# Kernel optimization log

Hardware: AMD Instinct MI355X
Metric: run time of the kernel (lower is better)

## Reference

```python
import jax, jax.numpy as jnp
import numpy as np

B, C, H, W, K = 8, 256, 128, 128, 9
P = K // 2
DN = ('NCHW', 'OIHW', 'NCHW')


def _dw(x, w, pad):
    # depthwise conv: w has shape (C,1,kh,kw), feature_group_count=C
    return jax.lax.conv_general_dilated(
        x, w, window_strides=(1, 1), padding=pad,
        dimension_numbers=DN, feature_group_count=C)


def setup_inputs() -> dict:
    key = jax.random.key(0)
    ks = jax.random.split(key, 6)
    s = 1.0 / np.sqrt(K)
    return {
        'x': jax.random.normal(ks[0], (B, C, H, W), dtype=jnp.float32),
        'wh1': jax.random.normal(ks[1], (C, 1, 1, K), dtype=jnp.float32) * s,
        'wh2': jax.random.normal(ks[2], (C, 1, 1, K), dtype=jnp.float32) * s,
        'wv1': jax.random.normal(ks[3], (C, 1, K, 1), dtype=jnp.float32) * s,
        'wv2': jax.random.normal(ks[4], (C, 1, K, 1), dtype=jnp.float32) * s,
        'wproj': jax.random.normal(ks[5], (C, 4 * C), dtype=jnp.float32) / np.sqrt(4 * C),
    }


def reference(x, wh1, wh2, wv1, wv2, wproj):
    pad_h = ((0, 0), (P, P))  # 1xK conv pads width
    pad_v = ((P, P), (0, 0))  # Kx1 conv pads height
    y = jnp.concatenate([
        _dw(x, wh1, pad_h),
        _dw(x, wh2, pad_h),
        _dw(x, wv1, pad_v),
        _dw(x, wv2, pad_v),
    ], axis=1)  # (B, 4C, H, W)
    out = jnp.einsum('oc,bchw->bohw', wproj, y)  # 1x1 projection
    return jax.nn.relu(out)
```

## Files before the change

### kernel.cpp

```cpp
#include <hip/hip_runtime.h>
#include <hip/hip_bf16.h>

#define BB 8
#define CC 256
#define HH 128
#define WW 128
#define KS 9
#define PADR 4
#define NPIX (BB*HH*WW)
#define KDIM (4*CC)

typedef __attribute__((ext_vector_type(8))) short bf16x8;
typedef __attribute__((ext_vector_type(4))) float f32x4;

static __device__ __forceinline__ unsigned short f2bf(float f) {
  union { float f; unsigned u; } v; v.f = f;
  unsigned r = v.u + 0x7FFF + ((v.u >> 16) & 1);
  return (unsigned short)(r >> 16);
}

__global__ void prep_kernel(const float* __restrict__ wproj,
                            unsigned short* __restrict__ Ap) {
  int idx = blockIdx.x * 256 + threadIdx.x;
  int o  = idx >> 10;
  int kp = idx & 1023;
  int c  = kp >> 2;
  int t  = kp & 3;
  Ap[idx] = f2bf(wproj[o * 1024 + t * 256 + c]);
}

__global__ __launch_bounds__(256)
void conv_kernel(const float* __restrict__ x,
                 const float* __restrict__ wh1, const float* __restrict__ wh2,
                 const float* __restrict__ wv1, const float* __restrict__ wv2,
                 unsigned short* __restrict__ Y) {
  int bid = blockIdx.x;
  int ht  = bid & 7;
  int bc  = bid >> 3;
  int c   = bc & 255;
  int tid = threadIdx.x;
  int hh  = tid >> 4;
  int w0  = (tid & 15) * 8;
  int h   = ht * 16 + hh;

  float swh1[KS], swh2[KS], swv1[KS], swv2[KS];
#pragma unroll
  for (int k = 0; k < KS; ++k) {
    swh1[k] = wh1[c * KS + k];
    swh2[k] = wh2[c * KS + k];
    swv1[k] = wv1[c * KS + k];
    swv2[k] = wv2[c * KS + k];
  }

  const float* xc = x + (size_t)bc * (HH * WW);

  float hw[16];
  {
    const float* xrow = xc + h * WW;
#pragma unroll
    for (int s = 0; s < 4; ++s) {
      int wb = w0 - 4 + s * 4;
      float4 seg;
      if (wb >= 0 && wb <= WW - 4) seg = *(const float4*)(xrow + wb);
      else seg = make_float4(0.f, 0.f, 0.f, 0.f);
      hw[s*4+0] = seg.x; hw[s*4+1] = seg.y; hw[s*4+2] = seg.z; hw[s*4+3] = seg.w;
    }
  }

  float vv[KS][8];
#pragma unroll
  for (int k = 0; k < KS; ++k) {
    int r = h + k - PADR;
    if (r >= 0 && r < HH) {
      const float* rp = xc + r * WW + w0;
      float4 a = *(const float4*)(rp);
      float4 b4 = *(const float4*)(rp + 4);
      vv[k][0]=a.x; vv[k][1]=a.y; vv[k][2]=a.z; vv[k][3]=a.w;
      vv[k][4]=b4.x; vv[k][5]=b4.y; vv[k][6]=b4.z; vv[k][7]=b4.w;
    } else {
#pragma unroll
      for (int j = 0; j < 8; ++j) vv[k][j] = 0.f;
    }
  }

  int b = bc >> 8;
  size_t ybase = ((size_t)((b * HH + h) * WW + w0)) * KDIM + (size_t)c * 4;

#pragma unroll
  for (int w = 0; w < 8; ++w) {
    float s1 = 0.f, s2 = 0.f, s3 = 0.f, s4 = 0.f;
#pragma unroll
    for (int k = 0; k < KS; ++k) {
      float xh = hw[w + k];
      s1 = fmaf(xh, swh1[k], s1);
      s2 = fmaf(xh, swh2[k], s2);
      float xv = vv[k][w];
      s3 = fmaf(xv, swv1[k], s3);
      s4 = fmaf(xv, swv2[k], s4);
    }
    unsigned u0 = (unsigned)f2bf(s1) | ((unsigned)f2bf(s2) << 16);
    unsigned u1 = (unsigned)f2bf(s3) | ((unsigned)f2bf(s4) << 16);
    *(uint2*)(Y + ybase + (size_t)w * KDIM) = make_uint2(u0, u1);
  }
}

__global__ __launch_bounds__(512)
void gemm_kernel(const unsigned short* __restrict__ Ap,
                 const unsigned short* __restrict__ Yg,
                 float* __restrict__ out) {
  int bid  = blockIdx.x;
  int tid  = threadIdx.x;
  int lane = tid & 63;
  int wv   = tid >> 6;
  int wm   = wv & 3;
  int wn   = wv >> 2;
  int l15  = lane & 15;
  int kseg = lane >> 4;

  const short* A = (const short*)Ap;
  const short* Yb = (const short*)Yg;

  f32x4 acc[4][4] = {};

  size_t abase = (size_t)(wm * 64 + l15) * KDIM + kseg * 8;
  size_t bbase = ((size_t)bid * 128 + wn * 64 + l15) * KDIM + kseg * 8;

  for (int k0 = 0; k0 < KDIM; k0 += 32) {
    bf16x8 a[4], bfr[4];
#pragma unroll
    for (int m = 0; m < 4; ++m)
      a[m] = *(const bf16x8*)(A + abase + (size_t)m * 16 * KDIM + k0);
#pragma unroll
    for (int n = 0; n < 4; ++n)
      bfr[n] = *(const bf16x8*)(Yb + bbase + (size_t)n * 16 * KDIM + k0);
#pragma unroll
    for (int m = 0; m < 4; ++m)
#pragma unroll
      for (int n = 0; n < 4; ++n)
        acc[m][n] = __builtin_amdgcn_mfma_f32_16x16x32_bf16(a[m], bfr[n],
                                                            acc[m][n], 0, 0, 0);
  }

  int b    = bid >> 7;
  int hrow = bid & 127;
#pragma unroll
  for (int m = 0; m < 4; ++m) {
#pragma unroll
    for (int n = 0; n < 4; ++n) {
#pragma unroll
      for (int r = 0; r < 4; ++r) {
        int o = wm * 64 + m * 16 + kseg * 4 + r;
        int w = wn * 64 + n * 16 + l15;
        out[((size_t)(b * 256 + o) << 14) + (hrow << 7) + w] =
            fmaxf(acc[m][n][r], 0.f);
      }
    }
  }
}

extern "C" void kernel_launch(void* const* d_in, const int* in_sizes, int n_in,
                              void* d_out, int out_size, void* d_ws, size_t ws_size,
                              hipStream_t stream) {
  (void)in_sizes; (void)n_in; (void)out_size; (void)ws_size;
  const float* x     = (const float*)d_in[0];
  const float* wh1   = (const float*)d_in[1];
  const float* wh2   = (const float*)d_in[2];
  const float* wv1   = (const float*)d_in[3];
  const float* wv2   = (const float*)d_in[4];
  const float* wproj = (const float*)d_in[5];
  float* out = (float*)d_out;

  unsigned short* Yg = (unsigned short*)d_ws;
  unsigned short* Ap = (unsigned short*)((char*)d_ws
                        + (size_t)NPIX * KDIM * sizeof(unsigned short));

  hipLaunchKernelGGL(prep_kernel, dim3(KDIM * CC / 256), dim3(256), 0, stream,
                     wproj, Ap);
  hipLaunchKernelGGL(conv_kernel, dim3(BB * CC * (HH / 16)), dim3(256), 0, stream,
                     x, wh1, wh2, wv1, wv2, Yg);
  hipLaunchKernelGGL(gemm_kernel, dim3(BB * HH), dim3(512), 0, stream,
                     Ap, Yg, out);
}
```

Baseline: 655.3 us.

## Stage GEMM tiles in LDS via direct loads and remap conv to channel-per-thread

The GEMM now stages 128x64 bf16 tiles of the weights and activations into shared memory with global_load_lds and splits the output channels into two tiles, giving 256-thread blocks and twice as many blocks. Block IDs are swizzled so that neighbouring blocks land on different XCDs. The conv kernel now runs one thread per channel and walks a whole row, so each thread's writes cover 4 contiguous bf16 values for one pixel. This is meant to make the Y stores coalesce across channels, where the old per-pixel scattered 8-byte writes did not. The trade-off is strided x reads across channels in the conv and fewer, longer-running conv blocks.

```diff
diff --git a/kernel.cpp b/kernel.cpp
--- a/kernel.cpp
+++ b/kernel.cpp
@@ -19,6 +19,12 @@
   return (unsigned short)(r >> 16);
 }
 
+static __device__ __forceinline__ void gload_lds16(const void* g, void* l) {
+  __builtin_amdgcn_global_load_lds(
+      (const __attribute__((address_space(1))) void*)g,
+      (__attribute__((address_space(3))) void*)l, 16, 0, 0);
+}
+
 __global__ void prep_kernel(const float* __restrict__ wproj,
                             unsigned short* __restrict__ Ap) {
   int idx = blockIdx.x * 256 + threadIdx.x;
@@ -35,123 +41,134 @@
                  const float* __restrict__ wv1, const float* __restrict__ wv2,
                  unsigned short* __restrict__ Y) {
   int bid = blockIdx.x;
-  int ht  = bid & 7;
-  int bc  = bid >> 3;
-  int c   = bc & 255;
-  int tid = threadIdx.x;
-  int hh  = tid >> 4;
-  int w0  = (tid & 15) * 8;
-  int h   = ht * 16 + hh;
-
-  float swh1[KS], swh2[KS], swv1[KS], swv2[KS];
+  bid = (bid & 7) * 128 + (bid >> 3);
+  int h = bid & 127;
+  int c = threadIdx.x;
+
+  float W1[KS], W2[KS], W3[KS], W4[KS];
 #pragma unroll
   for (int k = 0; k < KS; ++k) {
-    swh1[k] = wh1[c * KS + k];
-    swh2[k] = wh2[c * KS + k];
-    swv1[k] = wv1[c * KS + k];
-    swv2[k] = wv2[c * KS + k];
-  }
-
-  const float* xc = x + (size_t)bc * (HH * WW);
-
-  float hw[16];
-  {
-    const float* xrow = xc + h * WW;
-#pragma unroll
-    for (int s = 0; s < 4; ++s) {
-      int wb = w0 - 4 + s * 4;
-      float4 seg;
-      if (wb >= 0 && wb <= WW - 4) seg = *(const float4*)(xrow + wb);
-      else seg = make_float4(0.f, 0.f, 0.f, 0.f);
-      hw[s*4+0] = seg.x; hw[s*4+1] = seg.y; hw[s*4+2] = seg.z; hw[s*4+3] = seg.w;
-    }
-  }
-
-  float vv[KS][8];
-#pragma unroll
-  for (int k = 0; k < KS; ++k) {
-    int r = h + k - PADR;
-    if (r >= 0 && r < HH) {
-      const float* rp = xc + r * WW + w0;
-      float4 a = *(const float4*)(rp);
-      float4 b4 = *(const float4*)(rp + 4);
-      vv[k][0]=a.x; vv[k][1]=a.y; vv[k][2]=a.z; vv[k][3]=a.w;
-      vv[k][4]=b4.x; vv[k][5]=b4.y; vv[k][6]=b4.z; vv[k][7]=b4.w;
-    } else {
-#pragma unroll
-      for (int j = 0; j < 8; ++j) vv[k][j] = 0.f;
-    }
-  }
-
-  int b = bc >> 8;
-  size_t ybase = ((size_t)((b * HH + h) * WW + w0)) * KDIM + (size_t)c * 4;
-
-#pragma unroll
-  for (int w = 0; w < 8; ++w) {
-    float s1 = 0.f, s2 = 0.f, s3 = 0.f, s4 = 0.f;
+    W1[k] = wh1[c * KS + k];
+    W2[k] = wh2[c * KS + k];
+    W3[k] = wv1[c * KS + k];
+    W4[k] = wv2[c * KS + k];
+  }
+
+  int b = bid >> 7;
+  const float* xc = x + ((size_t)(b * CC + c)) * (HH * WW);
+  unsigned short* yrow = Y + (size_t)bid * 128 * KDIM + (size_t)c * 4;
+
+  for (int w0 = 0; w0 < WW; w0 += 8) {
+    float hw[16];
+    {
+      const float* xr = xc + h * WW;
+#pragma unroll
+      for (int s = 0; s < 4; ++s) {
+        int wb = w0 - 4 + s * 4;
+        float4 seg;
+        if (wb >= 0 && wb <= WW - 4) seg = *(const float4*)(xr + wb);
+        else seg = make_float4(0.f, 0.f, 0.f, 0.f);
+        hw[s*4+0]=seg.x; hw[s*4+1]=seg.y; hw[s*4+2]=seg.z; hw[s*4+3]=seg.w;
+      }
+    }
+    float vv[KS][8];
 #pragma unroll
     for (int k = 0; k < KS; ++k) {
-      float xh = hw[w + k];
-      s1 = fmaf(xh, swh1[k], s1);
-      s2 = fmaf(xh, swh2[k], s2);
-      float xv = vv[k][w];
-      s3 = fmaf(xv, swv1[k], s3);
-      s4 = fmaf(xv, swv2[k], s4);
-    }
-    unsigned u0 = (unsigned)f2bf(s1) | ((unsigned)f2bf(s2) << 16);
-    unsigned u1 = (unsigned)f2bf(s3) | ((unsigned)f2bf(s4) << 16);
-    *(uint2*)(Y + ybase + (size_t)w * KDIM) = make_uint2(u0, u1);
-  }
-}
-
-__global__ __launch_bounds__(512)
+      int r = h + k - PADR;
+      if (r >= 0 && r < HH) {
+        const float* rp = xc + r * WW + w0;
+        float4 a = *(const float4*)(rp);
+        float4 b4 = *(const float4*)(rp + 4);
+        vv[k][0]=a.x; vv[k][1]=a.y; vv[k][2]=a.z; vv[k][3]=a.w;
+        vv[k][4]=b4.x; vv[k][5]=b4.y; vv[k][6]=b4.z; vv[k][7]=b4.w;
+      } else {
+#pragma unroll
+        for (int j = 0; j < 8; ++j) vv[k][j] = 0.f;
+      }
+    }
+#pragma unroll
+    for (int w = 0; w < 8; ++w) {
+      float s1 = 0.f, s2 = 0.f, s3 = 0.f, s4 = 0.f;
+#pragma unroll
+      for (int k = 0; k < KS; ++k) {
+        float xh = hw[w + k];
+        s1 = fmaf(xh, W1[k], s1);
+        s2 = fmaf(xh, W2[k], s2);
+        float xv = vv[k][w];
+        s3 = fmaf(xv, W3[k], s3);
+        s4 = fmaf(xv, W4[k], s4);
+      }
+      unsigned u0 = (unsigned)f2bf(s1) | ((unsigned)f2bf(s2) << 16);
+      unsigned u1 = (unsigned)f2bf(s3) | ((unsigned)f2bf(s4) << 16);
+      *(uint2*)(yrow + (size_t)(w0 + w) * KDIM) = make_uint2(u0, u1);
+    }
+  }
+}
+
+__global__ __launch_bounds__(256)
 void gemm_kernel(const unsigned short* __restrict__ Ap,
                  const unsigned short* __restrict__ Yg,
                  float* __restrict__ out) {
-  int bid  = blockIdx.x;
-  int tid  = threadIdx.x;
-  int lane = tid & 63;
-  int wv   = tid >> 6;
-  int wm   = wv & 3;
-  int wn   = wv >> 2;
-  int l15  = lane & 15;
-  int kseg = lane >> 4;
-
-  const short* A = (const short*)Ap;
-  const short* Yb = (const short*)Yg;
+  __shared__ short As[128 * 64];
+  __shared__ short Bs[128 * 64];
+
+  int bid = blockIdx.x;
+  bid = (bid & 7) * 256 + (bid >> 3);
+  int otile = bid & 1;
+  int pt    = bid >> 1;
+  int tid   = threadIdx.x;
+  int lane  = tid & 63;
+  int wv    = tid >> 6;
+  int om    = wv & 1;
+  int pn    = wv >> 1;
+  int l15   = lane & 15;
+  int kseg  = lane >> 4;
+
+  const short* A  = (const short*)Ap + (size_t)(otile * 128) * KDIM;
+  const short* Bg = (const short*)Yg + (size_t)pt * 128 * KDIM;
+
+  int srow = tid >> 3;
+  int skc  = (tid & 7) * 8;
 
   f32x4 acc[4][4] = {};
 
-  size_t abase = (size_t)(wm * 64 + l15) * KDIM + kseg * 8;
-  size_t bbase = ((size_t)bid * 128 + wn * 64 + l15) * KDIM + kseg * 8;
-
-  for (int k0 = 0; k0 < KDIM; k0 += 32) {
-    bf16x8 a[4], bfr[4];
-#pragma unroll
-    for (int m = 0; m < 4; ++m)
-      a[m] = *(const bf16x8*)(A + abase + (size_t)m * 16 * KDIM + k0);
-#pragma unroll
-    for (int n = 0; n < 4; ++n)
-      bfr[n] = *(const bf16x8*)(Yb + bbase + (size_t)n * 16 * KDIM + k0);
-#pragma unroll
-    for (int m = 0; m < 4; ++m)
+  for (int k0 = 0; k0 < KDIM; k0 += 64) {
+#pragma unroll
+    for (int i = 0; i < 4; ++i) {
+      int rr = i * 32 + srow;
+      gload_lds16(A  + (size_t)rr * KDIM + k0 + skc, &As[rr * 64 + skc]);
+      gload_lds16(Bg + (size_t)rr * KDIM + k0 + skc, &Bs[rr * 64 + skc]);
+    }
+    __syncthreads();
+#pragma unroll
+    for (int kk = 0; kk < 2; ++kk) {
+      bf16x8 af[4], bfr[4];
+#pragma unroll
+      for (int m = 0; m < 4; ++m)
+        af[m] = *(const bf16x8*)&As[(om * 64 + m * 16 + l15) * 64 + kk * 32 + kseg * 8];
 #pragma unroll
       for (int n = 0; n < 4; ++n)
-        acc[m][n] = __builtin_amdgcn_mfma_f32_16x16x32_bf16(a[m], bfr[n],
-                                                            acc[m][n], 0, 0, 0);
-  }
-
-  int b    = bid >> 7;
-  int hrow = bid & 127;
+        bfr[n] = *(const bf16x8*)&Bs[(pn * 64 + n * 16 + l15) * 64 + kk * 32 + kseg * 8];
+#pragma unroll
+      for (int m = 0; m < 4; ++m)
+#pragma unroll
+        for (int n = 0; n < 4; ++n)
+          acc[m][n] = __builtin_amdgcn_mfma_f32_16x16x32_bf16(af[m], bfr[n],
+                                                              acc[m][n], 0, 0, 0);
+    }
+    __syncthreads();
+  }
+
+  int b = pt >> 7, h = pt & 127;
 #pragma unroll
   for (int m = 0; m < 4; ++m) {
 #pragma unroll
     for (int n = 0; n < 4; ++n) {
 #pragma unroll
       for (int r = 0; r < 4; ++r) {
-        int o = wm * 64 + m * 16 + kseg * 4 + r;
-        int w = wn * 64 + n * 16 + l15;
-        out[((size_t)(b * 256 + o) << 14) + (hrow << 7) + w] =
+        int o = otile * 128 + om * 64 + m * 16 + kseg * 4 + r;
+        int w = pn * 64 + n * 16 + l15;
+        out[((size_t)(b * 256 + o) << 14) + (h << 7) + w] =
             fmaxf(acc[m][n][r], 0.f);
       }
     }
@@ -176,8 +193,8 @@
 
   hipLaunchKernelGGL(prep_kernel, dim3(KDIM * CC / 256), dim3(256), 0, stream,
                      wproj, Ap);
-  hipLaunchKernelGGL(conv_kernel, dim3(BB * CC * (HH / 16)), dim3(256), 0, stream,
+  hipLaunchKernelGGL(conv_kernel, dim3(BB * HH), dim3(256), 0, stream,
                      x, wh1, wh2, wv1, wv2, Yg);
-  hipLaunchKernelGGL(gemm_kernel, dim3(BB * HH), dim3(512), 0, stream,
+  hipLaunchKernelGGL(gemm_kernel, dim3(2 * BB * HH), dim3(512 / 2), 0, stream,
                      Ap, Yg, out);
 }
```

Measured after the change: 553.8 us. 15.5% less time.
